# Kernel tuning notes

Hardware: AMD Instinct MI355X
Metric: run time of the kernel (lower is better)

## Reference

```python
import jax, jax.numpy as jnp
import numpy as np

D_IN = 4096
D_OUT = 4096
EPS_NORM = 1e-6
EPS_Q = 1e-8


def _ternary_quantize(w):
    # per-output-channel absmean scale, then round/clamp to {-1,0,1}
    gamma = jnp.mean(jnp.abs(w), axis=-1)
    w_q = jnp.clip(jnp.round(w / (gamma[:, None] + EPS_Q)), -1.0, 1.0)
    return w_q, gamma


def setup_inputs() -> dict:
    key = jax.random.key(0)
    kx, kw = jax.random.split(key)
    x = jax.random.normal(kx, (2, 4096, D_IN), dtype=jnp.float32)
    # kaiming-uniform-like init then ternarize (mirrors torch __init__)
    bound = 1.0 / np.sqrt(D_IN)
    w_init = jax.random.uniform(kw, (D_OUT, D_IN), minval=-bound, maxval=bound, dtype=jnp.float32)
    w_q, gamma = _ternary_quantize(w_init)
    norm_weight = jnp.ones((D_IN,), dtype=jnp.float32)
    return {"x": x, "norm_weight": norm_weight, "w_q": w_q, "gamma": gamma}


def reference(x, norm_weight, w_q, gamma):
    # RMSNorm
    rms = jnp.sqrt(jnp.mean(x * x, axis=-1, keepdims=True) + EPS_NORM)
    xn = x / rms * norm_weight
    # ternary linear (dense fp32 GEMM, math identical to F.linear) + per-channel scale
    y = jnp.einsum('bsd,od->bso', xn, w_q) * gamma
    return y
```

## Files before the change

### kernel.cpp

```cpp
#include <hip/hip_runtime.h>
#include <hip/hip_bf16.h>
#include <stdint.h>

#define D_IN  4096
#define D_OUT 4096
#define MROWS 8192

using i32x4 = __attribute__((ext_vector_type(4))) int;

__global__ __launch_bounds__(256) void prep_kernel(
    const float* __restrict__ x, const float* __restrict__ nw,
    signed char* __restrict__ xq, float* __restrict__ srow,
    const float* __restrict__ wq, signed char* __restrict__ wb) {
  const int b = blockIdx.x;
  const int t = threadIdx.x;

  if (b < MROWS) {
    const float4* xr  = (const float4*)(x + (size_t)b * D_IN);
    const float4* nw4 = (const float4*)nw;

    float4 p[4];
    float ss = 0.f, mx = 0.f;
#pragma unroll
    for (int i = 0; i < 4; ++i) {
      const float4 v = xr[i * 256 + t];
      const float4 w = nw4[i * 256 + t];
      ss += v.x * v.x + v.y * v.y + v.z * v.z + v.w * v.w;
      p[i].x = v.x * w.x; p[i].y = v.y * w.y;
      p[i].z = v.z * w.z; p[i].w = v.w * w.w;
      mx = fmaxf(mx, fmaxf(fmaxf(fabsf(p[i].x), fabsf(p[i].y)),
                           fmaxf(fabsf(p[i].z), fabsf(p[i].w))));
    }
#pragma unroll
    for (int off = 32; off > 0; off >>= 1) {
      ss += __shfl_down(ss, off, 64);
      mx = fmaxf(mx, __shfl_down(mx, off, 64));
    }

    __shared__ float rs[4], rm[4];
    if ((t & 63) == 0) { rs[t >> 6] = ss; rm[t >> 6] = mx; }
    __syncthreads();
    const float scale =
        rsqrtf((rs[0] + rs[1] + rs[2] + rs[3]) * (1.0f / D_IN) + 1e-6f);
    const float rowmax = fmaxf(fmaxf(rm[0], rm[1]), fmaxf(rm[2], rm[3])) * scale;
    const float s   = fmaxf(rowmax, 1e-20f) * (1.0f / 127.0f);
    const float f   = scale / s;
    if (t == 0) srow[b] = s;

    int* out = (int*)(xq + (size_t)b * D_IN);
#pragma unroll
    for (int i = 0; i < 4; ++i) {
      const int q0 = (int)rintf(p[i].x * f);
      const int q1 = (int)rintf(p[i].y * f);
      const int q2 = (int)rintf(p[i].z * f);
      const int q3 = (int)rintf(p[i].w * f);
      out[i * 256 + t] =
          (q0 & 0xFF) | ((q1 & 0xFF) << 8) | ((q2 & 0xFF) << 16) | (q3 << 24);
    }
  } else {
    const int cb = b - MROWS;
    const float4* w4 = (const float4*)wq;
    int* o = (int*)wb;
#pragma unroll
    for (int i = 0; i < 4; ++i) {
      const int idx = cb * 1024 + i * 256 + t;
      const float4 v = w4[idx];
      const int q0 = (int)v.x, q1 = (int)v.y, q2 = (int)v.z, q3 = (int)v.w;
      o[idx] = (q0 & 0xFF) | ((q1 & 0xFF) << 8) | ((q2 & 0xFF) << 16) | (q3 << 24);
    }
  }
}

#define BM 256
#define BN 256
#define BKB 64
#define NKT (D_IN / BKB)
#define SLOT_BYTES (BM * BKB)

#define WVM(n_) asm volatile("s_waitcnt vmcnt(" #n_ ")" ::: "memory")
#define BAR()   __builtin_amdgcn_s_barrier()

#define STAGE(t_, s_)                                                         \
  do {                                                                        \
    const int _k0 = (t_) * BKB;                                               \
    _Pragma("unroll") for (int _i = 0; _i < 2; ++_i)                          \
        __builtin_amdgcn_global_load_lds(                                     \
            (__attribute__((address_space(1))) void*)(A + aOff[_i] + _k0),    \
            (__attribute__((address_space(3))) void*)&sA[s_][ldsOff[_i]],     \
            16, 0, 0);                                                        \
    _Pragma("unroll") for (int _i = 0; _i < 2; ++_i)                          \
        __builtin_amdgcn_global_load_lds(                                     \
            (__attribute__((address_space(1))) void*)(B + bOff[_i] + _k0),    \
            (__attribute__((address_space(3))) void*)&sB[s_][ldsOff[_i]],     \
            16, 0, 0);                                                        \
  } while (0)

#define COMPUTE(s_)                                                           \
  do {                                                                        \
    i32x4 af[8], bfr[4];                                                      \
    _Pragma("unroll") for (int _i = 0; _i < 8; ++_i)                          \
        af[_i] = *(const i32x4*)&sA[s_][aoff + _i * (16 * BKB)];              \
    _Pragma("unroll") for (int _j = 0; _j < 4; ++_j)                          \
        bfr[_j] = *(const i32x4*)&sB[s_][boff + _j * (16 * BKB)];             \
    __builtin_amdgcn_s_setprio(1);                                            \
    _Pragma("unroll") for (int _i = 0; _i < 8; ++_i)                          \
        _Pragma("unroll") for (int _j = 0; _j < 4; ++_j)                      \
            acc[_i][_j] = __builtin_amdgcn_mfma_i32_16x16x64_i8(              \
                af[_i], bfr[_j], acc[_i][_j], 0, 0, 0);                       \
    __builtin_amdgcn_s_setprio(0);                                            \
  } while (0)

__global__ __launch_bounds__(512, 2) void gemm_kernel(
    const signed char* __restrict__ A,
    const signed char* __restrict__ B,
    const float* __restrict__ srow,
    const float* __restrict__ gamma,
    float* __restrict__ C) {
  __shared__ __align__(16) signed char sA[4][SLOT_BYTES];
  __shared__ __align__(16) signed char sB[4][SLOT_BYTES];

  const int tid  = threadIdx.x;
  const int lane = tid & 63;
  const int wv   = tid >> 6;
  const int wm   = wv >> 2;
  const int wn   = wv & 3;
  const int bn   = blockIdx.x;
  const int bm   = blockIdx.y;

  i32x4 acc[8][4];
#pragma unroll
  for (int i = 0; i < 8; ++i)
#pragma unroll
    for (int j = 0; j < 4; ++j) acc[i][j] = (i32x4){0, 0, 0, 0};

  size_t aOff[2], bOff[2];
  int ldsOff[2];
#pragma unroll
  for (int i = 0; i < 2; ++i) {
    const int c  = i * 512 + tid;
    const int r  = c >> 2;
    const int cc = ((c & 3) ^ ((r >> 1) & 3)) * 16;
    aOff[i] = (size_t)(bm * BM + r) * D_IN + cc;
    bOff[i] = (size_t)(bn * BN + r) * D_IN + cc;
    ldsOff[i] = (i * 512 + wv * 64) * 16;
  }

  const int kk   = (((lane >> 4) ^ ((lane >> 1) & 3))) * 16;
  const int aoff = (wm * 128 + (lane & 15)) * BKB + kk;
  const int boff = (wn * 64  + (lane & 15)) * BKB + kk;

  STAGE(0, 0);
  STAGE(1, 1);
  STAGE(2, 2);
  WVM(8);
  BAR();

#pragma unroll 1
  for (int t4 = 0; t4 < NKT - 4; t4 += 4) {
    STAGE(t4 + 3, 3); COMPUTE(0); WVM(8); BAR();
    STAGE(t4 + 4, 0); COMPUTE(1); WVM(8); BAR();
    STAGE(t4 + 5, 1); COMPUTE(2); WVM(8); BAR();
    STAGE(t4 + 6, 2); COMPUTE(3); WVM(8); BAR();
  }
  STAGE(NKT - 1, 3); COMPUTE(0); WVM(8); BAR();
  COMPUTE(1); WVM(4); BAR();
  COMPUTE(2); WVM(0); BAR();
  COMPUTE(3);

  const int col0 = bn * BN + wn * 64 + (lane & 15);
  const int row0 = bm * BM + wm * 128 + ((lane >> 4) * 4);
  float g[4];
#pragma unroll
  for (int j = 0; j < 4; ++j) g[j] = gamma[col0 + j * 16];

#pragma unroll
  for (int i = 0; i < 8; ++i) {
#pragma unroll
    for (int r = 0; r < 4; ++r) {
      const int row = row0 + i * 16 + r;
      const float sr = srow[row];
#pragma unroll
      for (int j = 0; j < 4; ++j) {
        C[(size_t)row * D_OUT + col0 + j * 16] =
            (float)acc[i][j][r] * sr * g[j];
      }
    }
  }
}

#undef STAGE
#undef COMPUTE
#undef WVM
#undef BAR

extern "C" void kernel_launch(void* const* d_in, const int* in_sizes, int n_in,
                              void* d_out, int out_size, void* d_ws, size_t ws_size,
                              hipStream_t stream) {
  const float* x     = (const float*)d_in[0];
  const float* nw    = (const float*)d_in[1];
  const float* wq    = (const float*)d_in[2];
  const float* gamma = (const float*)d_in[3];
  float* y = (float*)d_out;

  signed char* xq = (signed char*)d_ws;
  signed char* wb = xq + (size_t)MROWS * D_IN;
  float* srow = (float*)(wb + (size_t)D_OUT * D_IN);

  prep_kernel<<<MROWS + 4096, 256, 0, stream>>>(x, nw, xq, srow, wq, wb);

  gemm_kernel<<<dim3(D_OUT / BN, MROWS / BM), 512, 0, stream>>>(xq, wb, srow, gamma, y);
}
```

Baseline: 388.0 us.

## Double-buffer LDS fragment reads in registers to overlap with MFMA compute

Restructures the GEMM main loop so the LDS fragment reads for the next k-tile are issued before the MFMAs of the current tile, using two register fragment buffers. The wait counts are retuned so the next tile is resident before its early read. The goal is to hide LDS read latency behind matrix instructions. In exchange, register pressure rises with the extra fragment set, which could hurt at the 2-waves-per-EU launch bound, and the wait/barrier ordering becomes more delicate.

After: 384.2 us. Within noise of the previous version (-1.0%).

```diff
diff --git a/kernel.cpp b/kernel.cpp
--- a/kernel.cpp
+++ b/kernel.cpp
@@ -80,34 +80,49 @@
 #define WVM(n_) asm volatile("s_waitcnt vmcnt(" #n_ ")" ::: "memory")
 #define BAR()   __builtin_amdgcn_s_barrier()
 
-#define STAGE(t_, s_)                                                         \
-  do {                                                                        \
-    const int _k0 = (t_) * BKB;                                               \
+#define STAGE(t_)                                                             \
+  do {                                                                        \
     _Pragma("unroll") for (int _i = 0; _i < 2; ++_i)                          \
         __builtin_amdgcn_global_load_lds(                                     \
-            (__attribute__((address_space(1))) void*)(A + aOff[_i] + _k0),    \
-            (__attribute__((address_space(3))) void*)&sA[s_][ldsOff[_i]],     \
+            (__attribute__((address_space(1))) void*)(A + aOff[_i] +          \
+                                                      (t_) * BKB),            \
+            (__attribute__((address_space(3))) void*)&sA[(t_) & 3]            \
+                                                       [ldsOff[_i]],          \
             16, 0, 0);                                                        \
     _Pragma("unroll") for (int _i = 0; _i < 2; ++_i)                          \
         __builtin_amdgcn_global_load_lds(                                     \
-            (__attribute__((address_space(1))) void*)(B + bOff[_i] + _k0),    \
-            (__attribute__((address_space(3))) void*)&sB[s_][ldsOff[_i]],     \
+            (__attribute__((address_space(1))) void*)(B + bOff[_i] +          \
+                                                      (t_) * BKB),            \
+            (__attribute__((address_space(3))) void*)&sB[(t_) & 3]            \
+                                                       [ldsOff[_i]],          \
             16, 0, 0);                                                        \
   } while (0)
 
-#define COMPUTE(s_)                                                           \
-  do {                                                                        \
-    i32x4 af[8], bfr[4];                                                      \
+#define READF(t_, fa_, fb_)                                                   \
+  do {                                                                        \
     _Pragma("unroll") for (int _i = 0; _i < 8; ++_i)                          \
-        af[_i] = *(const i32x4*)&sA[s_][aoff + _i * (16 * BKB)];              \
+        fa_[_i] = *(const i32x4*)&sA[(t_) & 3][aoff0 + _i * (16 * BKB)];      \
     _Pragma("unroll") for (int _j = 0; _j < 4; ++_j)                          \
-        bfr[_j] = *(const i32x4*)&sB[s_][boff + _j * (16 * BKB)];             \
+        fb_[_j] = *(const i32x4*)&sB[(t_) & 3][boff0 + _j * (16 * BKB)];      \
+  } while (0)
+
+#define MFMA_C(fa_, fb_)                                                      \
+  do {                                                                        \
     __builtin_amdgcn_s_setprio(1);                                            \
     _Pragma("unroll") for (int _i = 0; _i < 8; ++_i)                          \
         _Pragma("unroll") for (int _j = 0; _j < 4; ++_j)                      \
             acc[_i][_j] = __builtin_amdgcn_mfma_i32_16x16x64_i8(              \
-                af[_i], bfr[_j], acc[_i][_j], 0, 0, 0);                       \
+                fa_[_i], fb_[_j], acc[_i][_j], 0, 0, 0);                      \
     __builtin_amdgcn_s_setprio(0);                                            \
+  } while (0)
+
+#define BODY(T_, fcA_, fcB_, fnA_, fnB_, STG_, WAIT_)                         \
+  do {                                                                        \
+    READF((T_) + 1, fnA_, fnB_);                                              \
+    STG_;                                                                     \
+    MFMA_C(fcA_, fcB_);                                                       \
+    WAIT_;                                                                    \
+    BAR();                                                                    \
   } while (0)
 
 __global__ __launch_bounds__(512, 2) void gemm_kernel(
@@ -145,27 +160,27 @@
     ldsOff[i] = (i * 512 + wv * 64) * 16;
   }
 
-  const int kk   = (((lane >> 4) ^ ((lane >> 1) & 3))) * 16;
-  const int aoff = (wm * 128 + (lane & 15)) * BKB + kk;
-  const int boff = (wn * 64  + (lane & 15)) * BKB + kk;
-
-  STAGE(0, 0);
-  STAGE(1, 1);
-  STAGE(2, 2);
-  WVM(8);
+  const int kk    = (((lane >> 4) ^ ((lane >> 1) & 3))) * 16;
+  const int aoff0 = (wm * 128 + (lane & 15)) * BKB + kk;
+  const int boff0 = (wn * 64  + (lane & 15)) * BKB + kk;
+
+  i32x4 f0a[8], f0b[4], f1a[8], f1b[4];
+
+  STAGE(0); STAGE(1); STAGE(2);
+  WVM(4);
   BAR();
+  READF(0, f0a, f0b);
 
 #pragma unroll 1
-  for (int t4 = 0; t4 < NKT - 4; t4 += 4) {
-    STAGE(t4 + 3, 3); COMPUTE(0); WVM(8); BAR();
-    STAGE(t4 + 4, 0); COMPUTE(1); WVM(8); BAR();
-    STAGE(t4 + 5, 1); COMPUTE(2); WVM(8); BAR();
-    STAGE(t4 + 6, 2); COMPUTE(3); WVM(8); BAR();
-  }
-  STAGE(NKT - 1, 3); COMPUTE(0); WVM(8); BAR();
-  COMPUTE(1); WVM(4); BAR();
-  COMPUTE(2); WVM(0); BAR();
-  COMPUTE(3);
+  for (int T = 0; T < NKT - 4; T += 2) {
+    BODY(T,     f0a, f0b, f1a, f1b, STAGE(T + 3), WVM(4));
+    BODY(T + 1, f1a, f1b, f0a, f0b, STAGE(T + 4), WVM(4));
+  }
+  BODY(60, f0a, f0b, f1a, f1b, STAGE(63), WVM(4));
+  BODY(61, f1a, f1b, f0a, f0b, ,          WVM(0));
+  READF(63, f1a, f1b);
+  MFMA_C(f0a, f0b);
+  MFMA_C(f1a, f1b);
 
   const int col0 = bn * BN + wn * 64 + (lane & 15);
   const int row0 = bm * BM + wm * 128 + ((lane >> 4) * 4);
@@ -188,8 +203,10 @@
   }
 }
 
+#undef BODY
+#undef MFMA_C
+#undef READF
 #undef STAGE
-#undef COMPUTE
 #undef WVM
 #undef BAR
 
```
